# Optimization experiments

Measured on AMD Instinct MI355X. Metric: run time of the kernel, lower is better.

Reference implementation:

```python
import jax, jax.numpy as jnp
import numpy as np

NEIGHBORS = 16  # init kwarg 'neighbors'


def _mlp(x, params):
    # SetTransform with reduction='none': pointwise MLP, ReLU between layers, linear output
    for W, b in params[:-1]:
        x = jax.nn.relu(x @ W + b)
    W, b = params[-1]
    return x @ W + b


def setup_inputs() -> dict:
    key = jax.random.key(0)
    B, K, P, DIM, C_IN = 4, 2048, 4096, 3, 64
    C_MID, C_OUT = 32, 128
    WH = 32          # weight_hidden sizes
    FH = 256         # final_hidden size
    FIN = C_IN * C_MID  # 2048, final_conv input

    ks = jax.random.split(key, 16)

    def lin(k, fan_in, fan_out):
        k1, k2 = jax.random.split(k)
        s = 1.0 / np.sqrt(fan_in)
        W = jax.random.uniform(k1, (fan_in, fan_out), minval=-s, maxval=s, dtype=jnp.float32)
        b = jax.random.uniform(k2, (fan_out,), minval=-s, maxval=s, dtype=jnp.float32)
        return W, b

    wc0_W, wc0_b = lin(ks[0], DIM, WH)
    wc1_W, wc1_b = lin(ks[1], WH, WH)
    wc2_W, wc2_b = lin(ks[2], WH, C_MID)
    fc0_W, fc0_b = lin(ks[3], FIN, FH)
    fc1_W, fc1_b = lin(ks[4], FH, C_OUT)

    return {
        "keys": jax.random.normal(ks[5], (B, K, DIM), dtype=jnp.float32),
        "points": jax.random.normal(ks[6], (B, P, DIM), dtype=jnp.float32),
        "feats": jax.random.normal(ks[7], (B, P, C_IN), dtype=jnp.float32),
        "wc0_W": wc0_W, "wc0_b": wc0_b,
        "wc1_W": wc1_W, "wc1_b": wc1_b,
        "wc2_W": wc2_W, "wc2_b": wc2_b,
        "fc0_W": fc0_W, "fc0_b": fc0_b,
        "fc1_W": fc1_W, "fc1_b": fc1_b,
    }


def reference(keys, points, feats,
              wc0_W, wc0_b, wc1_W, wc1_b, wc2_W, wc2_b,
              fc0_W, fc0_b, fc1_W, fc1_b):
    B, K, _ = keys.shape
    # Euclidean dist_fn: rel_pos [B,K,P,dim], squared dist [B,K,P]; all points valid
    dist_vec = points[:, None, :, :] - keys[:, :, None, :]
    dist = jnp.sum(dist_vec * dist_vec, axis=-1)
    # k smallest distances -> neighbor indices [B,K,N]
    _, idxs = jax.lax.top_k(-dist, NEIGHBORS)
    # gather relative positions [B,K,N,dim] and neighbor features [B,K,N,c_in]
    neighbor_rel = jnp.take_along_axis(dist_vec, idxs[..., None], axis=2)
    b_idx = jnp.arange(B)[:, None, None]
    neighbor_feats = feats[b_idx, idxs]
    # per-edge weight MLP: [B,K,N,dim] -> [B,K,N,c_mid]
    m = _mlp(neighbor_rel, [(wc0_W, wc0_b), (wc1_W, wc1_b), (wc2_W, wc2_b)])
    # masked matmul aggregation (all neighbors valid under euclidean dist_fn):
    # m^T @ neighbor_feats -> [B,K,c_mid,c_in], flattened to [B,K,c_mid*c_in]
    e = jnp.einsum('bknm,bknc->bkmc', m, neighbor_feats).reshape(B, K, -1)
    # final pointwise MLP -> [B,K,c_out]
    return _mlp(e, [(fc0_W, fc0_b), (fc1_W, fc1_b)])
```

## Files before the change

### kernel.cpp

```cpp
#include <hip/hip_runtime.h>
#include <cfloat>
#include <climits>

#define BATCH 4
#define KQ    2048
#define NP    4096
#define CIN   64
#define CMID  32
#define NB    16
#define NBINS 4096
#define CANDCAP 256
#define QPB   8

typedef short   bf16x8  __attribute__((ext_vector_type(8)));
typedef float   floatx4 __attribute__((ext_vector_type(4)));

__device__ __forceinline__ unsigned short f2bf(float f) {
  unsigned u = __float_as_uint(f);
  u = (u + 0x7fffu + ((u >> 16) & 1u)) >> 16;
  return (unsigned short)u;
}
__device__ __forceinline__ float bf2f(unsigned short u) {
  return __uint_as_float((unsigned)u << 16);
}

__device__ __forceinline__ void load_lds16(const void* g, void* l) {
  __builtin_amdgcn_global_load_lds(
      (const __attribute__((address_space(1))) unsigned int*)g,
      (__attribute__((address_space(3))) unsigned int*)l, 16, 0, 0);
}

__global__ __launch_bounds__(256) void select_topk(
    const float* __restrict__ keys, const float* __restrict__ points,
    int* __restrict__ nidx_g) {
  __shared__ int   hist[NBINS];
  __shared__ int   psum[256];
  __shared__ float cand_d[CANDCAP];
  __shared__ int   cand_i[CANDCAP];
  __shared__ int   nidx[NB];
  __shared__ int   sel_cnt, cand_cnt, sBin, sCbelow;

  const int tid = threadIdx.x;
  const int b   = blockIdx.x >> 11;

  for (int i = tid; i < NBINS; i += 256) hist[i] = 0;
  if (tid == 0) { sel_cnt = 0; cand_cnt = 0; }

  const float kx = keys[blockIdx.x * 3 + 0];
  const float ky = keys[blockIdx.x * 3 + 1];
  const float kz = keys[blockIdx.x * 3 + 2];
  __syncthreads();

  const float4* pv =
      reinterpret_cast<const float4*>(points + (size_t)b * NP * 3) + (size_t)tid * 12;
  float f[48];
#pragma unroll
  for (int c = 0; c < 12; ++c) {
    const float4 v = pv[c];
    f[c * 4 + 0] = v.x; f[c * 4 + 1] = v.y; f[c * 4 + 2] = v.z; f[c * 4 + 3] = v.w;
  }
  float dreg[16];
#pragma unroll
  for (int j = 0; j < 16; ++j) {
    const float dx = f[j * 3 + 0] - kx;
    const float dy = f[j * 3 + 1] - ky;
    const float dz = f[j * 3 + 2] - kz;
    const float d  = dx * dx + dy * dy + dz * dz;
    dreg[j] = d;
    atomicAdd(&hist[__float_as_uint(d) >> 19], 1);
  }
  __syncthreads();

  {
    const int base = tid * 16;
    int s = 0;
#pragma unroll
    for (int j = 0; j < 16; ++j) s += hist[base + j];
    psum[tid] = s;
  }
  __syncthreads();

  if (tid < 64) {
    const int q = psum[tid * 4] + psum[tid * 4 + 1] + psum[tid * 4 + 2] + psum[tid * 4 + 3];
    int incl = q;
#pragma unroll
    for (int off = 1; off < 64; off <<= 1) {
      int u = __shfl_up(incl, off);
      if (tid >= off) incl += u;
    }
    unsigned long long bal = __ballot(incl >= NB);
    int firstlane = __ffsll((long long)bal) - 1;
    if (tid == firstlane) {
      int cum = incl - q;
      int bin = -1;
      for (int t = 0; t < 4 && bin < 0; ++t) {
        const int ps = psum[tid * 4 + t];
        if (cum + ps >= NB) {
          const int b0 = (tid * 4 + t) * 16;
          for (int j = 0; j < 16; ++j) {
            const int h = hist[b0 + j];
            if (cum + h >= NB) { bin = b0 + j; break; }
            cum += h;
          }
        } else cum += ps;
      }
      sBin = bin; sCbelow = cum;
    }
  }
  __syncthreads();

  const unsigned B = (unsigned)sBin;
#pragma unroll
  for (int j = 0; j < 16; ++j) {
    const int i = tid * 16 + j;
    const unsigned bk = __float_as_uint(dreg[j]) >> 19;
    if (bk < B) {
      int pos = atomicAdd(&sel_cnt, 1);
      nidx[pos] = i;
    } else if (bk == B) {
      int pos = atomicAdd(&cand_cnt, 1);
      if (pos < CANDCAP) { cand_d[pos] = dreg[j]; cand_i[pos] = i; }
    }
  }
  __syncthreads();

  if (tid < 64) {
    const int rem = NB - sCbelow;
    const int cc  = min(cand_cnt, CANDCAP);
    for (int s = 0; s < rem; ++s) {
      float bd = FLT_MAX; int bi = INT_MAX; int bp = -1;
      for (int j = tid; j < cc; j += 64) {
        float d = cand_d[j]; int ii = cand_i[j];
        if (d < bd || (d == bd && ii < bi)) { bd = d; bi = ii; bp = j; }
      }
#pragma unroll
      for (int off = 32; off > 0; off >>= 1) {
        float od = __shfl_down(bd, off);
        int   oi = __shfl_down(bi, off);
        int   op = __shfl_down(bp, off);
        if (od < bd || (od == bd && oi < bi)) { bd = od; bi = oi; bp = op; }
      }
      if (tid == 0) { nidx[sCbelow + s] = bi; cand_d[bp] = FLT_MAX; }
    }
  }
  __syncthreads();

  if (tid < NB) nidx_g[blockIdx.x * NB + tid] = nidx[tid];
}

__global__ __launch_bounds__(256) void edge_prep(
    const float* __restrict__ keys, const float* __restrict__ points,
    const float* __restrict__ feats, const int* __restrict__ nidx_g,
    const float* __restrict__ wc0_W, const float* __restrict__ wc0_b,
    const float* __restrict__ wc1_W, const float* __restrict__ wc1_b,
    const float* __restrict__ wc2_W, const float* __restrict__ wc2_b,
    const float* __restrict__ fc0_W, const float* __restrict__ fc1_W,
    unsigned short* __restrict__ W0T, unsigned short* __restrict__ W1T,
    unsigned short* __restrict__ E) {
  __shared__ float w0[96], b0v[32], w1[1024], b1v[32], w2[1024], b2v[32];
  __shared__ int   idx_s[QPB * NB];
  __shared__ __align__(16) unsigned short m_bf[QPB * NB][40];
  __shared__ __align__(16) char u_mem[128 * 144];
  float (*h2_all)[33]        = reinterpret_cast<float(*)[33]>(u_mem);
  unsigned short (*f_bf)[72] = reinterpret_cast<unsigned short(*)[72]>(u_mem);
  float (*tt)[33]            = reinterpret_cast<float(*)[33]>(u_mem);

  const int tid = threadIdx.x;
  const int bid = blockIdx.x;
  const int q0  = bid * QPB;
  const int b   = q0 >> 11;

  if (bid < 544) {
    const float* W; unsigned short* WT; int K, N, k0, n0;
    if (bid < 512) { W = fc0_W; WT = W0T; K = 2048; N = 256;
                     k0 = (bid >> 3) * 32; n0 = (bid & 7) * 32; }
    else           { W = fc1_W; WT = W1T; K = 256;  N = 128;
                     k0 = ((bid - 512) >> 2) * 32; n0 = ((bid - 512) & 3) * 32; }
    const int tx = tid & 31, ty = tid >> 5;
#pragma unroll
    for (int p = 0; p < 4; ++p)
      tt[ty + p * 8][tx] = W[(size_t)(k0 + ty + p * 8) * N + n0 + tx];
    __syncthreads();
#pragma unroll
    for (int p = 0; p < 4; ++p)
      WT[(size_t)(n0 + ty + p * 8) * K + k0 + tx] = f2bf(tt[tx][ty + p * 8]);
    __syncthreads();
  }

  if (tid < 96) w0[tid] = wc0_W[tid];
  for (int i = tid; i < 1024; i += 256) { w1[i] = wc1_W[i]; w2[i] = wc2_W[i]; }
  if (tid < 32) { b0v[tid] = wc0_b[tid]; b1v[tid] = wc1_b[tid]; b2v[tid] = wc2_b[tid]; }
  if (tid < QPB * NB) idx_s[tid] = nidx_g[q0 * NB + tid];
  __syncthreads();

  const int edge = tid & 127;
  const int half = tid >> 7;
  const int ob   = half * 16;
  const int qe   = edge >> 4;
  const int idx  = idx_s[edge];
  {
    const float* p  = points + ((size_t)b * NP + idx) * 3;
    const float* kq = keys + (size_t)(q0 + qe) * 3;
    const float rx = p[0] - kq[0], ry = p[1] - kq[1], rz = p[2] - kq[2];

    float h1[32];
#pragma unroll
    for (int o = 0; o < 32; ++o)
      h1[o] = fmaxf(0.f, rx * w0[o] + ry * w0[32 + o] + rz * w0[64 + o] + b0v[o]);
#pragma unroll
    for (int j = 0; j < 16; ++j) {
      const int o = ob + j;
      float a = b1v[o];
#pragma unroll
      for (int i = 0; i < 32; ++i) a += h1[i] * w1[i * 32 + o];
      h2_all[edge][o] = fmaxf(a, 0.f);
    }
  }
  __syncthreads();

  float mo[16];
#pragma unroll
  for (int j = 0; j < 16; ++j) {
    const int o = ob + j;
    float a = b2v[o];
#pragma unroll
    for (int i = 0; i < 32; ++i) a += h2_all[edge][i] * w2[i * 32 + o];
    mo[j] = a;
  }
#pragma unroll
  for (int j = 0; j < 8; ++j) {
    const unsigned lo = f2bf(mo[2 * j]), hi = f2bf(mo[2 * j + 1]);
    *reinterpret_cast<unsigned*>(&m_bf[edge][ob + 2 * j]) = lo | (hi << 16);
  }
  __syncthreads();

#pragma unroll
  for (int t = 0; t < 8; ++t) {
    const int task = tid + t * 256;
    const int row = task >> 4, ch = task & 15;
    const float4 v = *reinterpret_cast<const float4*>(
        feats + ((size_t)b * NP + idx_s[row]) * CIN + ch * 4);
    ushort4 o4;
    o4.x = f2bf(v.x); o4.y = f2bf(v.y); o4.z = f2bf(v.z); o4.w = f2bf(v.w);
    *reinterpret_cast<ushort4*>(&f_bf[row][ch * 4]) = o4;
  }
  __syncthreads();

  const int wv = tid >> 6, lane = tid & 63;
  const int co = lane & 7, mg = lane >> 3;
#pragma unroll
  for (int it = 0; it < 2; ++it) {
    const int q = wv + it * 4;
    float acc[4][8] = {};
#pragma unroll
    for (int n = 0; n < 16; ++n) {
      const int row = q * 16 + n;
      const ushort4 m4 = *reinterpret_cast<const ushort4*>(&m_bf[row][mg * 4]);
      const float mv[4] = {bf2f(m4.x), bf2f(m4.y), bf2f(m4.z), bf2f(m4.w)};
      const uint4 fv = *reinterpret_cast<const uint4*>(&f_bf[row][co * 8]);
      float fc[8];
      fc[0] = __uint_as_float(fv.x << 16); fc[1] = __uint_as_float(fv.x & 0xffff0000u);
      fc[2] = __uint_as_float(fv.y << 16); fc[3] = __uint_as_float(fv.y & 0xffff0000u);
      fc[4] = __uint_as_float(fv.z << 16); fc[5] = __uint_as_float(fv.z & 0xffff0000u);
      fc[6] = __uint_as_float(fv.w << 16); fc[7] = __uint_as_float(fv.w & 0xffff0000u);
#pragma unroll
      for (int i = 0; i < 4; ++i)
#pragma unroll
        for (int j = 0; j < 8; ++j) acc[i][j] += mv[i] * fc[j];
    }
    unsigned short* Eq = E + (size_t)(q0 + q) * 2048;
#pragma unroll
    for (int i = 0; i < 4; ++i) {
      const int mid = mg * 4 + i;
      uint4 o;
      o.x = (unsigned)f2bf(acc[i][0]) | ((unsigned)f2bf(acc[i][1]) << 16);
      o.y = (unsigned)f2bf(acc[i][2]) | ((unsigned)f2bf(acc[i][3]) << 16);
      o.z = (unsigned)f2bf(acc[i][4]) | ((unsigned)f2bf(acc[i][5]) << 16);
      o.w = (unsigned)f2bf(acc[i][6]) | ((unsigned)f2bf(acc[i][7]) << 16);
      *reinterpret_cast<uint4*>(&Eq[mid * 64 + co * 8]) = o;
    }
  }
}

template <int KDIM, bool RELU, bool OUTBF16>
__global__ __launch_bounds__(256) void gemm_mfma(
    const unsigned short* __restrict__ A,
    const unsigned short* __restrict__ Bt,
    const float* __restrict__ bias,
    void* __restrict__ Cout, int ldc) {
  __shared__ __align__(16) unsigned short Al[64 * 128];
  __shared__ __align__(16) unsigned short Bl[64 * 128];
  const int tid  = threadIdx.x;
  const int m0   = blockIdx.x * 64, n0 = blockIdx.y * 64;
  const int wv   = tid >> 6, lane = tid & 63;
  const int quad = lane >> 4, s = lane & 15;
  const int moff = (wv & 1) * 32, noff = (wv >> 1) * 32;
  const int lr   = lane >> 4;
  const int lc   = lane & 15;

  floatx4 acc[2][2] = {{{0.f,0.f,0.f,0.f},{0.f,0.f,0.f,0.f}},
                       {{0.f,0.f,0.f,0.f},{0.f,0.f,0.f,0.f}}};

  for (int k0 = 0; k0 < KDIM; k0 += 128) {
#pragma unroll
    for (int t = 0; t < 4; ++t) {
      const int R0 = wv * 16 + t * 4;
      const int r  = R0 + lr;
      const int gc = lc ^ (r & 7);
      load_lds16(A  + (size_t)(m0 + r) * KDIM + k0 + gc * 8, &Al[R0 * 128]);
      load_lds16(Bt + (size_t)(n0 + r) * KDIM + k0 + gc * 8, &Bl[R0 * 128]);
    }
    __syncthreads();
#pragma unroll
    for (int h = 0; h < 4; ++h) {
      bf16x8 af[2], bfr[2];
#pragma unroll
      for (int i = 0; i < 2; ++i) {
        const int r = moff + i * 16 + s;
        af[i] = *reinterpret_cast<const bf16x8*>(
            &Al[(size_t)r * 128 + ((((h << 2) | quad) ^ (r & 7)) << 3)]);
      }
#pragma unroll
      for (int j = 0; j < 2; ++j) {
        const int r = noff + j * 16 + s;
        bfr[j] = *reinterpret_cast<const bf16x8*>(
            &Bl[(size_t)r * 128 + ((((h << 2) | quad) ^ (r & 7)) << 3)]);
      }
#pragma unroll
      for (int i = 0; i < 2; ++i)
#pragma unroll
        for (int j = 0; j < 2; ++j)
          acc[i][j] = __builtin_amdgcn_mfma_f32_16x16x32_bf16(af[i], bfr[j], acc[i][j], 0, 0, 0);
    }
    __syncthreads();
  }

#pragma unroll
  for (int i = 0; i < 2; ++i)
#pragma unroll
    for (int j = 0; j < 2; ++j) {
      const int col = n0 + noff + j * 16 + s;
      const float bv = bias[col];
#pragma unroll
      for (int r = 0; r < 4; ++r) {
        const int row = m0 + moff + i * 16 + quad * 4 + r;
        float v = acc[i][j][r] + bv;
        if (RELU) v = fmaxf(v, 0.f);
        if (OUTBF16)
          ((unsigned short*)Cout)[(size_t)row * ldc + col] = f2bf(v);
        else
          ((float*)Cout)[(size_t)row * ldc + col] = v;
      }
    }
}

extern "C" void kernel_launch(void* const* d_in, const int* in_sizes, int n_in,
                              void* d_out, int out_size, void* d_ws, size_t ws_size,
                              hipStream_t stream) {
  const float* keys   = (const float*)d_in[0];
  const float* points = (const float*)d_in[1];
  const float* feats  = (const float*)d_in[2];
  const float* wc0_W  = (const float*)d_in[3];
  const float* wc0_b  = (const float*)d_in[4];
  const float* wc1_W  = (const float*)d_in[5];
  const float* wc1_b  = (const float*)d_in[6];
  const float* wc2_W  = (const float*)d_in[7];
  const float* wc2_b  = (const float*)d_in[8];
  const float* fc0_W  = (const float*)d_in[9];
  const float* fc0_b  = (const float*)d_in[10];
  const float* fc1_W  = (const float*)d_in[11];
  const float* fc1_b  = (const float*)d_in[12];
  float* out = (float*)d_out;

  const int M = BATCH * KQ;
  char* ws = (char*)d_ws;
  unsigned short* E    = (unsigned short*)(ws);
  unsigned short* H16  = (unsigned short*)(ws + (size_t)33554432);
  unsigned short* W0T  = (unsigned short*)(ws + (size_t)37748736);
  unsigned short* W1T  = (unsigned short*)(ws + (size_t)38797312);
  int*            nidx = (int*)(ws + (size_t)38862848);

  select_topk<<<M, 256, 0, stream>>>(keys, points, nidx);
  edge_prep<<<M / QPB, 256, 0, stream>>>(keys, points, feats, nidx,
                                         wc0_W, wc0_b, wc1_W, wc1_b, wc2_W, wc2_b,
                                         fc0_W, fc1_W, W0T, W1T, E);
  gemm_mfma<2048, true,  true ><<<dim3(M / 64, 4), 256, 0, stream>>>(E, W0T, fc0_b, H16, 256);
  gemm_mfma<256,  false, false><<<dim3(M / 64, 2), 256, 0, stream>>>(H16, W1T, fc1_b, out, 128);
}
```

Measured before the change: 180.7 us.

## Fuse top-k selection and per-edge MLP aggregation into one kernel

Merges the neighbor-selection kernel and the edge-prep kernel so each block handles one query end to end: it selects the 16 neighbors, runs the weight MLP, gathers features and writes the aggregated row of E. This drops the global round-trip of neighbor indices and one kernel launch. In exchange, every one of the 8192 blocks now reloads the 8 KB of wc weights into shared memory, work per block drops from 8 queries to 1, and shared memory use per block rises, which could lower occupancy of the selection phase.

```diff
diff --git a/kernel.cpp b/kernel.cpp
--- a/kernel.cpp
+++ b/kernel.cpp
@@ -10,7 +10,6 @@
 #define NB    16
 #define NBINS 4096
 #define CANDCAP 256
-#define QPB   8
 
 typedef short   bf16x8  __attribute__((ext_vector_type(8)));
 typedef float   floatx4 __attribute__((ext_vector_type(4)));
@@ -30,25 +29,61 @@
       (__attribute__((address_space(3))) unsigned int*)l, 16, 0, 0);
 }
 
-__global__ __launch_bounds__(256) void select_topk(
+__global__ __launch_bounds__(256) void select_edge(
     const float* __restrict__ keys, const float* __restrict__ points,
-    int* __restrict__ nidx_g) {
-  __shared__ int   hist[NBINS];
+    const float* __restrict__ feats,
+    const float* __restrict__ wc0_W, const float* __restrict__ wc0_b,
+    const float* __restrict__ wc1_W, const float* __restrict__ wc1_b,
+    const float* __restrict__ wc2_W, const float* __restrict__ wc2_b,
+    const float* __restrict__ fc0_W, const float* __restrict__ fc1_W,
+    unsigned short* __restrict__ W0T, unsigned short* __restrict__ W1T,
+    unsigned short* __restrict__ E) {
+  __shared__ __align__(16) char uni[NBINS * 4];
+  int*   hist = reinterpret_cast<int*>(uni);
+  float (*tt)[33] = reinterpret_cast<float(*)[33]>(uni);
+  float (*h2_all)[33] = reinterpret_cast<float(*)[33]>(uni);
+  unsigned short (*m_bf)[34] =
+      reinterpret_cast<unsigned short(*)[34]>(uni + 2112);
+  unsigned short (*f_bf)[72] =
+      reinterpret_cast<unsigned short(*)[72]>(uni + 3200);
+
   __shared__ int   psum[256];
   __shared__ float cand_d[CANDCAP];
   __shared__ int   cand_i[CANDCAP];
   __shared__ int   nidx[NB];
   __shared__ int   sel_cnt, cand_cnt, sBin, sCbelow;
+  __shared__ float w0[96], b0v[32], w1[1024], b1v[32], w2[1024], b2v[32];
 
   const int tid = threadIdx.x;
-  const int b   = blockIdx.x >> 11;
-
+  const int bid = blockIdx.x;
+  const int b   = bid >> 11;
+
+  if (bid < 544) {
+    const float* W; unsigned short* WT; int K, N, k0, n0;
+    if (bid < 512) { W = fc0_W; WT = W0T; K = 2048; N = 256;
+                     k0 = (bid >> 3) * 32; n0 = (bid & 7) * 32; }
+    else           { W = fc1_W; WT = W1T; K = 256;  N = 128;
+                     k0 = ((bid - 512) >> 2) * 32; n0 = ((bid - 512) & 3) * 32; }
+    const int tx = tid & 31, ty = tid >> 5;
+#pragma unroll
+    for (int p = 0; p < 4; ++p)
+      tt[ty + p * 8][tx] = W[(size_t)(k0 + ty + p * 8) * N + n0 + tx];
+    __syncthreads();
+#pragma unroll
+    for (int p = 0; p < 4; ++p)
+      WT[(size_t)(n0 + ty + p * 8) * K + k0 + tx] = f2bf(tt[tx][ty + p * 8]);
+    __syncthreads();
+  }
+
+  if (tid < 96) w0[tid] = wc0_W[tid];
+  for (int i = tid; i < 1024; i += 256) { w1[i] = wc1_W[i]; w2[i] = wc2_W[i]; }
+  if (tid < 32) { b0v[tid] = wc0_b[tid]; b1v[tid] = wc1_b[tid]; b2v[tid] = wc2_b[tid]; }
   for (int i = tid; i < NBINS; i += 256) hist[i] = 0;
   if (tid == 0) { sel_cnt = 0; cand_cnt = 0; }
 
-  const float kx = keys[blockIdx.x * 3 + 0];
-  const float ky = keys[blockIdx.x * 3 + 1];
-  const float kz = keys[blockIdx.x * 3 + 2];
+  const float kx = keys[bid * 3 + 0];
+  const float ky = keys[bid * 3 + 1];
+  const float kz = keys[bid * 3 + 2];
   __syncthreads();
 
   const float4* pv =
@@ -145,140 +180,71 @@
   }
   __syncthreads();
 
-  if (tid < NB) nidx_g[blockIdx.x * NB + tid] = nidx[tid];
-}
-
-__global__ __launch_bounds__(256) void edge_prep(
-    const float* __restrict__ keys, const float* __restrict__ points,
-    const float* __restrict__ feats, const int* __restrict__ nidx_g,
-    const float* __restrict__ wc0_W, const float* __restrict__ wc0_b,
-    const float* __restrict__ wc1_W, const float* __restrict__ wc1_b,
-    const float* __restrict__ wc2_W, const float* __restrict__ wc2_b,
-    const float* __restrict__ fc0_W, const float* __restrict__ fc1_W,
-    unsigned short* __restrict__ W0T, unsigned short* __restrict__ W1T,
-    unsigned short* __restrict__ E) {
-  __shared__ float w0[96], b0v[32], w1[1024], b1v[32], w2[1024], b2v[32];
-  __shared__ int   idx_s[QPB * NB];
-  __shared__ __align__(16) unsigned short m_bf[QPB * NB][40];
-  __shared__ __align__(16) char u_mem[128 * 144];
-  float (*h2_all)[33]        = reinterpret_cast<float(*)[33]>(u_mem);
-  unsigned short (*f_bf)[72] = reinterpret_cast<unsigned short(*)[72]>(u_mem);
-  float (*tt)[33]            = reinterpret_cast<float(*)[33]>(u_mem);
-
-  const int tid = threadIdx.x;
-  const int bid = blockIdx.x;
-  const int q0  = bid * QPB;
-  const int b   = q0 >> 11;
-
-  if (bid < 544) {
-    const float* W; unsigned short* WT; int K, N, k0, n0;
-    if (bid < 512) { W = fc0_W; WT = W0T; K = 2048; N = 256;
-                     k0 = (bid >> 3) * 32; n0 = (bid & 7) * 32; }
-    else           { W = fc1_W; WT = W1T; K = 256;  N = 128;
-                     k0 = ((bid - 512) >> 2) * 32; n0 = ((bid - 512) & 3) * 32; }
-    const int tx = tid & 31, ty = tid >> 5;
-#pragma unroll
-    for (int p = 0; p < 4; ++p)
-      tt[ty + p * 8][tx] = W[(size_t)(k0 + ty + p * 8) * N + n0 + tx];
-    __syncthreads();
-#pragma unroll
-    for (int p = 0; p < 4; ++p)
-      WT[(size_t)(n0 + ty + p * 8) * K + k0 + tx] = f2bf(tt[tx][ty + p * 8]);
-    __syncthreads();
-  }
-
-  if (tid < 96) w0[tid] = wc0_W[tid];
-  for (int i = tid; i < 1024; i += 256) { w1[i] = wc1_W[i]; w2[i] = wc2_W[i]; }
-  if (tid < 32) { b0v[tid] = wc0_b[tid]; b1v[tid] = wc1_b[tid]; b2v[tid] = wc2_b[tid]; }
-  if (tid < QPB * NB) idx_s[tid] = nidx_g[q0 * NB + tid];
-  __syncthreads();
-
-  const int edge = tid & 127;
-  const int half = tid >> 7;
-  const int ob   = half * 16;
-  const int qe   = edge >> 4;
-  const int idx  = idx_s[edge];
+  const int e  = tid & 15;
+  const int o2 = tid >> 4;
+  const int idx = nidx[e];
   {
-    const float* p  = points + ((size_t)b * NP + idx) * 3;
-    const float* kq = keys + (size_t)(q0 + qe) * 3;
-    const float rx = p[0] - kq[0], ry = p[1] - kq[1], rz = p[2] - kq[2];
-
+    const float* p = points + ((size_t)b * NP + idx) * 3;
+    const float rx = p[0] - kx, ry = p[1] - ky, rz = p[2] - kz;
     float h1[32];
 #pragma unroll
     for (int o = 0; o < 32; ++o)
       h1[o] = fmaxf(0.f, rx * w0[o] + ry * w0[32 + o] + rz * w0[64 + o] + b0v[o]);
 #pragma unroll
-    for (int j = 0; j < 16; ++j) {
-      const int o = ob + j;
+    for (int j = 0; j < 2; ++j) {
+      const int o = o2 * 2 + j;
       float a = b1v[o];
 #pragma unroll
       for (int i = 0; i < 32; ++i) a += h1[i] * w1[i * 32 + o];
-      h2_all[edge][o] = fmaxf(a, 0.f);
-    }
-  }
-  __syncthreads();
-
-  float mo[16];
-#pragma unroll
-  for (int j = 0; j < 16; ++j) {
-    const int o = ob + j;
-    float a = b2v[o];
-#pragma unroll
-    for (int i = 0; i < 32; ++i) a += h2_all[edge][i] * w2[i * 32 + o];
-    mo[j] = a;
-  }
-#pragma unroll
-  for (int j = 0; j < 8; ++j) {
-    const unsigned lo = f2bf(mo[2 * j]), hi = f2bf(mo[2 * j + 1]);
-    *reinterpret_cast<unsigned*>(&m_bf[edge][ob + 2 * j]) = lo | (hi << 16);
-  }
-  __syncthreads();
-
-#pragma unroll
-  for (int t = 0; t < 8; ++t) {
-    const int task = tid + t * 256;
-    const int row = task >> 4, ch = task & 15;
+      h2_all[e][o] = fmaxf(a, 0.f);
+    }
+  }
+  __syncthreads();
+
+  {
+    float mo[2];
+#pragma unroll
+    for (int j = 0; j < 2; ++j) {
+      const int o = o2 * 2 + j;
+      float a = b2v[o];
+#pragma unroll
+      for (int i = 0; i < 32; ++i) a += h2_all[e][i] * w2[i * 32 + o];
+      mo[j] = a;
+    }
+    const unsigned lo = f2bf(mo[0]), hi = f2bf(mo[1]);
+    *reinterpret_cast<unsigned*>(&m_bf[e][o2 * 2]) = lo | (hi << 16);
+
+    const int row = tid >> 4, ch = tid & 15;
     const float4 v = *reinterpret_cast<const float4*>(
-        feats + ((size_t)b * NP + idx_s[row]) * CIN + ch * 4);
+        feats + ((size_t)b * NP + nidx[row]) * CIN + ch * 4);
     ushort4 o4;
     o4.x = f2bf(v.x); o4.y = f2bf(v.y); o4.z = f2bf(v.z); o4.w = f2bf(v.w);
     *reinterpret_cast<ushort4*>(&f_bf[row][ch * 4]) = o4;
   }
   __syncthreads();
 
-  const int wv = tid >> 6, lane = tid & 63;
-  const int co = lane & 7, mg = lane >> 3;
-#pragma unroll
-  for (int it = 0; it < 2; ++it) {
-    const int q = wv + it * 4;
-    float acc[4][8] = {};
+  {
+    const int mid = tid >> 3;
+    const int c0  = (tid & 7) * 8;
+    float acc[8] = {};
 #pragma unroll
     for (int n = 0; n < 16; ++n) {
-      const int row = q * 16 + n;
-      const ushort4 m4 = *reinterpret_cast<const ushort4*>(&m_bf[row][mg * 4]);
-      const float mv[4] = {bf2f(m4.x), bf2f(m4.y), bf2f(m4.z), bf2f(m4.w)};
-      const uint4 fv = *reinterpret_cast<const uint4*>(&f_bf[row][co * 8]);
+      const float mv = bf2f(m_bf[n][mid]);
+      const uint4 fv = *reinterpret_cast<const uint4*>(&f_bf[n][c0]);
       float fc[8];
       fc[0] = __uint_as_float(fv.x << 16); fc[1] = __uint_as_float(fv.x & 0xffff0000u);
       fc[2] = __uint_as_float(fv.y << 16); fc[3] = __uint_as_float(fv.y & 0xffff0000u);
       fc[4] = __uint_as_float(fv.z << 16); fc[5] = __uint_as_float(fv.z & 0xffff0000u);
       fc[6] = __uint_as_float(fv.w << 16); fc[7] = __uint_as_float(fv.w & 0xffff0000u);
 #pragma unroll
-      for (int i = 0; i < 4; ++i)
-#pragma unroll
-        for (int j = 0; j < 8; ++j) acc[i][j] += mv[i] * fc[j];
-    }
-    unsigned short* Eq = E + (size_t)(q0 + q) * 2048;
-#pragma unroll
-    for (int i = 0; i < 4; ++i) {
-      const int mid = mg * 4 + i;
-      uint4 o;
-      o.x = (unsigned)f2bf(acc[i][0]) | ((unsigned)f2bf(acc[i][1]) << 16);
-      o.y = (unsigned)f2bf(acc[i][2]) | ((unsigned)f2bf(acc[i][3]) << 16);
-      o.z = (unsigned)f2bf(acc[i][4]) | ((unsigned)f2bf(acc[i][5]) << 16);
-      o.w = (unsigned)f2bf(acc[i][6]) | ((unsigned)f2bf(acc[i][7]) << 16);
-      *reinterpret_cast<uint4*>(&Eq[mid * 64 + co * 8]) = o;
-    }
+      for (int j = 0; j < 8; ++j) acc[j] += mv * fc[j];
+    }
+    uint4 o;
+    o.x = (unsigned)f2bf(acc[0]) | ((unsigned)f2bf(acc[1]) << 16);
+    o.y = (unsigned)f2bf(acc[2]) | ((unsigned)f2bf(acc[3]) << 16);
+    o.z = (unsigned)f2bf(acc[4]) | ((unsigned)f2bf(acc[5]) << 16);
+    o.w = (unsigned)f2bf(acc[6]) | ((unsigned)f2bf(acc[7]) << 16);
+    *reinterpret_cast<uint4*>(&E[(size_t)bid * 2048 + mid * 64 + c0]) = o;
   }
 }
 
@@ -378,12 +344,10 @@
   unsigned short* H16  = (unsigned short*)(ws + (size_t)33554432);
   unsigned short* W0T  = (unsigned short*)(ws + (size_t)37748736);
   unsigned short* W1T  = (unsigned short*)(ws + (size_t)38797312);
-  int*            nidx = (int*)(ws + (size_t)38862848);
-
-  select_topk<<<M, 256, 0, stream>>>(keys, points, nidx);
-  edge_prep<<<M / QPB, 256, 0, stream>>>(keys, points, feats, nidx,
-                                         wc0_W, wc0_b, wc1_W, wc1_b, wc2_W, wc2_b,
-                                         fc0_W, fc1_W, W0T, W1T, E);
+
+  select_edge<<<M, 256, 0, stream>>>(keys, points, feats,
+                                     wc0_W, wc0_b, wc1_W, wc1_b, wc2_W, wc2_b,
+                                     fc0_W, fc1_W, W0T, W1T, E);
   gemm_mfma<2048, true,  true ><<<dim3(M / 64, 4), 256, 0, stream>>>(E, W0T, fc0_b, H16, 256);
   gemm_mfma<256,  false, false><<<dim3(M / 64, 2), 256, 0, stream>>>(H16, W1T, fc1_b, out, 128);
 }
```

Result: slower. 192.0 us (+6.2%).

## Rewrite top-k selection as a single wavefront per query with a coarser histogram

Applied to the files above, without the earlier changes.

The neighbor selection kernel now runs one 64-lane wavefront per query instead of a 256-thread block. Each lane computes distances for 64 points. The histogram drops to 1024 bins, keyed on fewer mantissa bits, and its prefix scan happens in registers with wave shuffles, removing most block-wide barriers and the separate partial-sum pass. Definitely selected indices go straight to global memory. The trade-offs are higher per-lane register pressure (64 distances held in registers), less parallelism per query, and more points landing in the threshold bin. Those threshold-bin points go into a candidate buffer that shrinks to 128 entries, which raises the risk of overflow.

```diff
diff --git a/kernel.cpp b/kernel.cpp
--- a/kernel.cpp
+++ b/kernel.cpp
@@ -8,8 +8,8 @@
 #define CIN   64
 #define CMID  32
 #define NB    16
-#define NBINS 4096
-#define CANDCAP 256
+#define SBINS 1024
+#define SCAND 128
 #define QPB   8
 
 typedef short   bf16x8  __attribute__((ext_vector_type(8)));
@@ -30,122 +30,119 @@
       (__attribute__((address_space(3))) unsigned int*)l, 16, 0, 0);
 }
 
-__global__ __launch_bounds__(256) void select_topk(
+__global__ __launch_bounds__(64, 4) void select_topk(
     const float* __restrict__ keys, const float* __restrict__ points,
     int* __restrict__ nidx_g) {
-  __shared__ int   hist[NBINS];
-  __shared__ int   psum[256];
-  __shared__ float cand_d[CANDCAP];
-  __shared__ int   cand_i[CANDCAP];
-  __shared__ int   nidx[NB];
-  __shared__ int   sel_cnt, cand_cnt, sBin, sCbelow;
-
-  const int tid = threadIdx.x;
-  const int b   = blockIdx.x >> 11;
-
-  for (int i = tid; i < NBINS; i += 256) hist[i] = 0;
-  if (tid == 0) { sel_cnt = 0; cand_cnt = 0; }
-
-  const float kx = keys[blockIdx.x * 3 + 0];
-  const float ky = keys[blockIdx.x * 3 + 1];
-  const float kz = keys[blockIdx.x * 3 + 2];
+  __shared__ int   hist[SBINS];
+  __shared__ float cand_d[SCAND];
+  __shared__ int   cand_i[SCAND];
+  __shared__ int   cnts[2];
+
+  const int lane = threadIdx.x;
+  const int q    = blockIdx.x;
+  const int b    = q >> 11;
+
+#pragma unroll
+  for (int t = 0; t < 4; ++t)
+    *reinterpret_cast<int4*>(&hist[(lane + t * 64) * 4]) = int4{0, 0, 0, 0};
+  if (lane < 2) cnts[lane] = 0;
+
+  const float kx = keys[q * 3 + 0];
+  const float ky = keys[q * 3 + 1];
+  const float kz = keys[q * 3 + 2];
   __syncthreads();
 
   const float4* pv =
-      reinterpret_cast<const float4*>(points + (size_t)b * NP * 3) + (size_t)tid * 12;
-  float f[48];
-#pragma unroll
-  for (int c = 0; c < 12; ++c) {
-    const float4 v = pv[c];
-    f[c * 4 + 0] = v.x; f[c * 4 + 1] = v.y; f[c * 4 + 2] = v.z; f[c * 4 + 3] = v.w;
-  }
-  float dreg[16];
-#pragma unroll
-  for (int j = 0; j < 16; ++j) {
-    const float dx = f[j * 3 + 0] - kx;
-    const float dy = f[j * 3 + 1] - ky;
-    const float dz = f[j * 3 + 2] - kz;
-    const float d  = dx * dx + dy * dy + dz * dz;
-    dreg[j] = d;
-    atomicAdd(&hist[__float_as_uint(d) >> 19], 1);
-  }
-  __syncthreads();
-
+      reinterpret_cast<const float4*>(points + (size_t)b * NP * 3) + (size_t)lane * 48;
+  float dreg[64];
+#pragma unroll
+  for (int g = 0; g < 4; ++g) {
+    float f[48];
+#pragma unroll
+    for (int c = 0; c < 12; ++c) {
+      const float4 v = pv[g * 12 + c];
+      f[c * 4 + 0] = v.x; f[c * 4 + 1] = v.y; f[c * 4 + 2] = v.z; f[c * 4 + 3] = v.w;
+    }
+#pragma unroll
+    for (int j = 0; j < 16; ++j) {
+      const float dx = f[j * 3 + 0] - kx;
+      const float dy = f[j * 3 + 1] - ky;
+      const float dz = f[j * 3 + 2] - kz;
+      const float d  = dx * dx + dy * dy + dz * dz;
+      dreg[g * 16 + j] = d;
+      atomicAdd(&hist[__float_as_uint(d) >> 21], 1);
+    }
+  }
+  __syncthreads();
+
+  int h[16]; int s = 0;
   {
-    const int base = tid * 16;
-    int s = 0;
-#pragma unroll
-    for (int j = 0; j < 16; ++j) s += hist[base + j];
-    psum[tid] = s;
-  }
-  __syncthreads();
-
-  if (tid < 64) {
-    const int q = psum[tid * 4] + psum[tid * 4 + 1] + psum[tid * 4 + 2] + psum[tid * 4 + 3];
-    int incl = q;
-#pragma unroll
-    for (int off = 1; off < 64; off <<= 1) {
-      int u = __shfl_up(incl, off);
-      if (tid >= off) incl += u;
-    }
-    unsigned long long bal = __ballot(incl >= NB);
-    int firstlane = __ffsll((long long)bal) - 1;
-    if (tid == firstlane) {
-      int cum = incl - q;
-      int bin = -1;
-      for (int t = 0; t < 4 && bin < 0; ++t) {
-        const int ps = psum[tid * 4 + t];
-        if (cum + ps >= NB) {
-          const int b0 = (tid * 4 + t) * 16;
-          for (int j = 0; j < 16; ++j) {
-            const int h = hist[b0 + j];
-            if (cum + h >= NB) { bin = b0 + j; break; }
-            cum += h;
-          }
-        } else cum += ps;
-      }
-      sBin = bin; sCbelow = cum;
-    }
-  }
-  __syncthreads();
-
-  const unsigned B = (unsigned)sBin;
-#pragma unroll
-  for (int j = 0; j < 16; ++j) {
-    const int i = tid * 16 + j;
-    const unsigned bk = __float_as_uint(dreg[j]) >> 19;
+    const int base = lane * 16;
+#pragma unroll
+    for (int t = 0; t < 4; ++t) {
+      const int4 hv = *reinterpret_cast<const int4*>(&hist[base + t * 4]);
+      h[t * 4 + 0] = hv.x; h[t * 4 + 1] = hv.y; h[t * 4 + 2] = hv.z; h[t * 4 + 3] = hv.w;
+      s += hv.x + hv.y + hv.z + hv.w;
+    }
+  }
+  int incl = s;
+#pragma unroll
+  for (int off = 1; off < 64; off <<= 1) {
+    const int u = __shfl_up(incl, off);
+    if (lane >= off) incl += u;
+  }
+  const unsigned long long bal = __ballot(incl >= NB);
+  const int fl = __ffsll((long long)bal) - 1;
+  int Bb = 0, cb = 0;
+  if (lane == fl) {
+    int cum = incl - s;
+    int bin = lane * 16;
+#pragma unroll
+    for (int j = 0; j < 16; ++j) {
+      if (cum + h[j] >= NB) { bin = lane * 16 + j; break; }
+      cum += h[j];
+    }
+    Bb = bin; cb = cum;
+  }
+  Bb = __shfl(Bb, fl);
+  cb = __shfl(cb, fl);
+
+  const unsigned B = (unsigned)Bb;
+#pragma unroll
+  for (int j = 0; j < 64; ++j) {
+    const unsigned bk = __float_as_uint(dreg[j]) >> 21;
+    const int i = lane * 64 + j;
     if (bk < B) {
-      int pos = atomicAdd(&sel_cnt, 1);
-      nidx[pos] = i;
+      const int pos = atomicAdd(&cnts[0], 1);
+      nidx_g[(size_t)q * NB + pos] = i;
     } else if (bk == B) {
-      int pos = atomicAdd(&cand_cnt, 1);
-      if (pos < CANDCAP) { cand_d[pos] = dreg[j]; cand_i[pos] = i; }
-    }
-  }
-  __syncthreads();
-
-  if (tid < 64) {
-    const int rem = NB - sCbelow;
-    const int cc  = min(cand_cnt, CANDCAP);
-    for (int s = 0; s < rem; ++s) {
-      float bd = FLT_MAX; int bi = INT_MAX; int bp = -1;
-      for (int j = tid; j < cc; j += 64) {
-        float d = cand_d[j]; int ii = cand_i[j];
-        if (d < bd || (d == bd && ii < bi)) { bd = d; bi = ii; bp = j; }
-      }
-#pragma unroll
-      for (int off = 32; off > 0; off >>= 1) {
-        float od = __shfl_down(bd, off);
-        int   oi = __shfl_down(bi, off);
-        int   op = __shfl_down(bp, off);
-        if (od < bd || (od == bd && oi < bi)) { bd = od; bi = oi; bp = op; }
-      }
-      if (tid == 0) { nidx[sCbelow + s] = bi; cand_d[bp] = FLT_MAX; }
-    }
-  }
-  __syncthreads();
-
-  if (tid < NB) nidx_g[blockIdx.x * NB + tid] = nidx[tid];
+      const int pos = atomicAdd(&cnts[1], 1);
+      if (pos < SCAND) { cand_d[pos] = dreg[j]; cand_i[pos] = i; }
+    }
+  }
+  __syncthreads();
+
+  const int rem = NB - cb;
+  const int cc  = min(cnts[1], SCAND);
+  for (int s2 = 0; s2 < rem; ++s2) {
+    float bd = FLT_MAX; int bi = INT_MAX; int bp = -1;
+    for (int j = lane; j < cc; j += 64) {
+      const float d = cand_d[j]; const int ii = cand_i[j];
+      if (d < bd || (d == bd && ii < bi)) { bd = d; bi = ii; bp = j; }
+    }
+#pragma unroll
+    for (int off = 32; off > 0; off >>= 1) {
+      const float od = __shfl_down(bd, off);
+      const int   oi = __shfl_down(bi, off);
+      const int   op = __shfl_down(bp, off);
+      if (od < bd || (od == bd && oi < bi)) { bd = od; bi = oi; bp = op; }
+    }
+    if (lane == 0) {
+      nidx_g[(size_t)q * NB + cb + s2] = bi;
+      cand_d[bp] = FLT_MAX;
+    }
+    __syncthreads();
+  }
 }
 
 __global__ __launch_bounds__(256) void edge_prep(
@@ -380,7 +377,7 @@
   unsigned short* W1T  = (unsigned short*)(ws + (size_t)38797312);
   int*            nidx = (int*)(ws + (size_t)38862848);
 
-  select_topk<<<M, 256, 0, stream>>>(keys, points, nidx);
+  select_topk<<<M, 64, 0, stream>>>(keys, points, nidx);
   edge_prep<<<M / QPB, 256, 0, stream>>>(keys, points, feats, nidx,
                                          wc0_W, wc0_b, wc1_W, wc1_b, wc2_W, wc2_b,
                                          fc0_W, fc1_W, W0T, W1T, E);
```

Measured after the change: 204.5 us. 1.13x slower.
